# Kernel tuning notes

Measured on AMD Instinct MI355X. Metric: run time of the kernel, lower is better.

## Reference

```python
import jax, jax.numpy as jnp
import numpy as np

B, NX, NC, D, H = 2, 512, 4096, 1024, 16
HD = D // H  # head_dim = context_dim // heads
LN_EPS = 1e-5


def setup_inputs() -> dict:
    key = jax.random.key(0)
    k0, k1, k2, k3, k4 = jax.random.split(key, 5)
    x = jax.random.normal(k0, (B, NX, D), dtype=jnp.float32)
    c = jax.random.normal(k1, (B, NC, D), dtype=jnp.float32)
    attn_mask = jax.random.randint(k2, (B, NX, NC), 0, 2).astype(bool)
    # learned params
    ln_w = jnp.ones((D,), jnp.float32)
    ln_b = jnp.zeros((D,), jnp.float32)
    Wq = jax.random.normal(k3, (D, D), dtype=jnp.float32) * 0.02  # to_q (query_dim -> inner_dim)
    Wo = jax.random.normal(k4, (D, D), dtype=jnp.float32) * 0.02  # to_out (inner_dim -> query_dim)
    return {"x": x, "c": c, "attn_mask": attn_mask, "ln_w": ln_w, "ln_b": ln_b, "Wq": Wq, "Wo": Wo}


def _layernorm(x, w, b):
    mu = jnp.mean(x, axis=-1, keepdims=True)
    var = jnp.mean(jnp.square(x - mu), axis=-1, keepdims=True)
    return (x - mu) * jax.lax.rsqrt(var + LN_EPS) * w + b


def reference(x, c, attn_mask, ln_w, ln_b, Wq, Wo):
    scale = HD ** (-0.5)
    xn = _layernorm(x, ln_w, ln_b)
    q = (xn @ Wq).reshape(B, NX, H, HD).transpose(0, 2, 1, 3)      # (B,H,NX,HD)
    kv0 = c.reshape(B, NC, H, HD).transpose(0, 2, 1, 3)             # (B,H,NC,HD) -- kvt=(kv0,kv0)
    kv = jnp.concatenate([q, kv0], axis=2)                          # kv_append_q=True -> (B,H,NX+NC,HD)
    # mask: ones for the appended-q block, user mask for context block
    m = jnp.broadcast_to(attn_mask[:, None, :, :], (B, H, NX, NC))
    full_mask = jnp.concatenate([jnp.ones((B, H, NX, NX), bool), m], axis=-1)
    sim = jnp.einsum('bhqd,bhkd->bhqk', q * scale, kv)              # (B,H,NX,NX+NC)
    neg = -jnp.finfo(sim.dtype).max
    sim = jnp.where(full_mask, sim, neg)
    attn = jax.nn.softmax(sim, axis=-1)
    a = jnp.einsum('bhqk,bhkd->bhqd', attn, kv)
    o = a.transpose(0, 2, 1, 3).reshape(B, NX, H * HD) @ Wo
    return (o, kv0)
```

## Files before the change

### kernel.cpp

```cpp
#include <hip/hip_runtime.h>

#define B_  2
#define NX_ 512
#define NC_ 4096
#define D_  1024
#define H_  16
#define HD_ 64
#define NT_ (NX_ + NC_)
#define NSPLIT 4
#define KBS (NT_ / 64 / NSPLIT)

typedef float  floatx4  __attribute__((ext_vector_type(4)));
typedef __bf16 bf16x8   __attribute__((ext_vector_type(8)));
typedef unsigned short ushort8v __attribute__((ext_vector_type(8)));

__device__ __forceinline__ bf16x8 as_bf16x8(ushort8v u) {
    union { ushort8v u; bf16x8 b; } c; c.u = u; return c.b;
}
__device__ __forceinline__ unsigned short f2bf(float f) {
    unsigned u = __float_as_uint(f);
    u += 0x7FFF + ((u >> 16) & 1);
    return (unsigned short)(u >> 16);
}

__global__ __launch_bounds__(256)
void prep_kernel(const float* __restrict__ x, const float* __restrict__ lw,
                 const float* __restrict__ lb, const float* __restrict__ Wq,
                 const float* __restrict__ Wo, const int* __restrict__ mask,
                 const float* __restrict__ c,
                 unsigned short* __restrict__ xnb, unsigned short* __restrict__ WqT,
                 unsigned short* __restrict__ WoT, unsigned* __restrict__ bits,
                 unsigned short* __restrict__ cbf, float* __restrict__ gz) {
    int blk = blockIdx.x;
    int tid = threadIdx.x;
    if (blk < 1024) {
        int row = blk;
        float4 v = reinterpret_cast<const float4*>(x)[(size_t)row * (D_ / 4) + tid];
        float s  = v.x + v.y + v.z + v.w;
        float s2 = v.x * v.x + v.y * v.y + v.z * v.z + v.w * v.w;
        #pragma unroll
        for (int off = 32; off > 0; off >>= 1) {
            s  += __shfl_down(s, off);
            s2 += __shfl_down(s2, off);
        }
        __shared__ float sm[4], sm2[4], stat[2];
        int wv = tid >> 6;
        if ((tid & 63) == 0) { sm[wv] = s; sm2[wv] = s2; }
        __syncthreads();
        if (tid == 0) {
            float S  = sm[0] + sm[1] + sm[2] + sm[3];
            float S2 = sm2[0] + sm2[1] + sm2[2] + sm2[3];
            float mu  = S * (1.0f / D_);
            float var = fmaxf(S2 * (1.0f / D_) - mu * mu, 0.0f);
            stat[0] = mu;
            stat[1] = rsqrtf(var + 1e-5f);
        }
        __syncthreads();
        float mu = stat[0], rs = stat[1];
        float4 w4 = reinterpret_cast<const float4*>(lw)[tid];
        float4 b4 = reinterpret_cast<const float4*>(lb)[tid];
        ushort4 o;
        o.x = f2bf((v.x - mu) * rs * w4.x + b4.x);
        o.y = f2bf((v.y - mu) * rs * w4.y + b4.y);
        o.z = f2bf((v.z - mu) * rs * w4.z + b4.z);
        o.w = f2bf((v.w - mu) * rs * w4.w + b4.w);
        reinterpret_cast<ushort4*>(xnb)[(size_t)row * (D_ / 4) + tid] = o;
    } else if (blk < 1536) {
        int which = (blk - 1024) >> 8;
        int t = (blk - 1024) & 255;
        const float* W = which ? Wo : Wq;
        unsigned short* WT = which ? WoT : WqT;
        __shared__ unsigned short T[64][72];
        int row0 = (t >> 4) * 64, col0 = (t & 15) * 64;
        int r = tid >> 2, ch = (tid & 3) * 16;
        const float* src = W + (size_t)(row0 + r) * D_ + col0 + ch;
        unsigned short vals[16];
        #pragma unroll
        for (int k = 0; k < 4; ++k) {
            float4 v = reinterpret_cast<const float4*>(src)[k];
            vals[k*4+0] = f2bf(v.x); vals[k*4+1] = f2bf(v.y);
            vals[k*4+2] = f2bf(v.z); vals[k*4+3] = f2bf(v.w);
        }
        #pragma unroll
        for (int i = 0; i < 16; ++i) T[ch + i][r] = vals[i];
        __syncthreads();
        unsigned short* dst = WT + (size_t)(col0 + r) * D_ + row0 + ch;
        uint4 o0 = *reinterpret_cast<uint4*>(&T[r][ch]);
        uint4 o1 = *reinterpret_cast<uint4*>(&T[r][ch + 8]);
        *reinterpret_cast<uint4*>(dst)     = o0;
        *reinterpret_cast<uint4*>(dst + 8) = o1;
    } else if (blk < 2048) {
        size_t w = (size_t)(blk - 1536) * 256 + tid;
        const int* src = mask + w * 32;
        unsigned b = 0;
        #pragma unroll
        for (int k = 0; k < 8; ++k) {
            int4 v = reinterpret_cast<const int4*>(src)[k];
            b |= (v.x != 0 ? 1u : 0u) << (k * 4 + 0);
            b |= (v.y != 0 ? 1u : 0u) << (k * 4 + 1);
            b |= (v.z != 0 ? 1u : 0u) << (k * 4 + 2);
            b |= (v.w != 0 ? 1u : 0u) << (k * 4 + 3);
        }
        bits[w] = b;
    } else if (blk < 10240) {
        size_t i = ((size_t)(blk - 2048) * 256 + tid) * 4;
        float4 v = *reinterpret_cast<const float4*>(c + i);
        ushort4 o;
        o.x = f2bf(v.x); o.y = f2bf(v.y); o.z = f2bf(v.z); o.w = f2bf(v.w);
        *reinterpret_cast<ushort4*>(cbf + i) = o;
    } else {
        size_t i = ((size_t)(blk - 10240) * 256 + tid) * 4;
        float4 z = {0.f, 0.f, 0.f, 0.f};
        *reinterpret_cast<float4*>(gz + i) = z;
    }
}

__global__ __launch_bounds__(256)
void kv0_kernel(const float* __restrict__ c, float* __restrict__ out2) {
    size_t i = (size_t)blockIdx.x * 256 + threadIdx.x;
    int d4 = (int)(i & 15);
    size_t r = i >> 4;
    int n = (int)(r % NC_);
    size_t r2 = r / NC_;
    int h = (int)(r2 & (H_ - 1));
    int b = (int)(r2 >> 4);
    float4 v = *reinterpret_cast<const float4*>(c + ((size_t)(b * NC_ + n)) * D_ + h * HD_ + d4 * 4);
    reinterpret_cast<float4*>(out2)[i] = v;
}

__global__ __launch_bounds__(256)
void gemm_bt_kernel(const unsigned short* __restrict__ A, const unsigned short* __restrict__ BT,
                    unsigned short* __restrict__ Cb) {
    __shared__ unsigned short As[64][72];
    __shared__ unsigned short Bs[64][72];
    int tid = threadIdx.x;
    int lane = tid & 63, wave = tid >> 6;
    int m16 = lane & 15, g = lane >> 4, g8 = g * 8;
    int row0 = blockIdx.y * 64, col0 = blockIdx.x * 64;
    int r = tid >> 2, ch = (tid & 3) * 16;

    floatx4 acc[4];
    #pragma unroll
    for (int t = 0; t < 4; ++t) acc[t] = (floatx4){0.f, 0.f, 0.f, 0.f};

    for (int kc = 0; kc < 16; ++kc) {
        int k0 = kc * 64;
        const unsigned short* asrc = A  + (size_t)(row0 + r) * D_ + k0 + ch;
        const unsigned short* bsrc = BT + (size_t)(col0 + r) * D_ + k0 + ch;
        uint4 a0 = *reinterpret_cast<const uint4*>(asrc);
        uint4 a1 = *reinterpret_cast<const uint4*>(asrc + 8);
        uint4 b0 = *reinterpret_cast<const uint4*>(bsrc);
        uint4 b1 = *reinterpret_cast<const uint4*>(bsrc + 8);
        *reinterpret_cast<uint4*>(&As[r][ch])     = a0;
        *reinterpret_cast<uint4*>(&As[r][ch + 8]) = a1;
        *reinterpret_cast<uint4*>(&Bs[r][ch])     = b0;
        *reinterpret_cast<uint4*>(&Bs[r][ch + 8]) = b1;
        __syncthreads();
        bf16x8 fa0 = as_bf16x8(*reinterpret_cast<ushort8v*>(&As[16 * wave + m16][g8]));
        bf16x8 fa1 = as_bf16x8(*reinterpret_cast<ushort8v*>(&As[16 * wave + m16][32 + g8]));
        #pragma unroll
        for (int t = 0; t < 4; ++t) {
            bf16x8 fb0 = as_bf16x8(*reinterpret_cast<ushort8v*>(&Bs[16 * t + m16][g8]));
            bf16x8 fb1 = as_bf16x8(*reinterpret_cast<ushort8v*>(&Bs[16 * t + m16][32 + g8]));
            acc[t] = __builtin_amdgcn_mfma_f32_16x16x32_bf16(fa0, fb0, acc[t], 0, 0, 0);
            acc[t] = __builtin_amdgcn_mfma_f32_16x16x32_bf16(fa1, fb1, acc[t], 0, 0, 0);
        }
        __syncthreads();
    }
    #pragma unroll
    for (int t = 0; t < 4; ++t)
        #pragma unroll
        for (int reg = 0; reg < 4; ++reg)
            Cb[(size_t)(row0 + 16 * wave + g * 4 + reg) * D_ + col0 + 16 * t + m16] = f2bf(acc[t][reg]);
}

__global__ __launch_bounds__(256)
void gemm_attn_kernel(const float* __restrict__ gacc, const float* __restrict__ gacc_l,
                      const unsigned short* __restrict__ BT, float* __restrict__ out) {
    __shared__ unsigned short As[64][72];
    __shared__ unsigned short Bs[64][72];
    int tid = threadIdx.x;
    int lane = tid & 63, wave = tid >> 6;
    int m16 = lane & 15, g = lane >> 4, g8 = g * 8;
    int row0 = blockIdx.y * 64, col0 = blockIdx.x * 64;
    int r = tid >> 2, ch = (tid & 3) * 16;

    floatx4 acc[4];
    #pragma unroll
    for (int t = 0; t < 4; ++t) acc[t] = (floatx4){0.f, 0.f, 0.f, 0.f};

    for (int kc = 0; kc < 16; ++kc) {
        int k0 = kc * 64;
        int row = row0 + r;
        float inv = 1.0f / fmaxf(gacc_l[(size_t)row * H_ + kc], 1e-35f);
        const float* asrc = gacc + (size_t)row * D_ + k0 + ch;
        const unsigned short* bsrc = BT + (size_t)(col0 + r) * D_ + k0 + ch;
        unsigned short av[16];
        #pragma unroll
        for (int t = 0; t < 4; ++t) {
            float4 v = reinterpret_cast<const float4*>(asrc)[t];
            av[t*4+0] = f2bf(v.x * inv); av[t*4+1] = f2bf(v.y * inv);
            av[t*4+2] = f2bf(v.z * inv); av[t*4+3] = f2bf(v.w * inv);
        }
        uint4 b0 = *reinterpret_cast<const uint4*>(bsrc);
        uint4 b1 = *reinterpret_cast<const uint4*>(bsrc + 8);
        *reinterpret_cast<uint4*>(&As[r][ch])     = *reinterpret_cast<uint4*>(&av[0]);
        *reinterpret_cast<uint4*>(&As[r][ch + 8]) = *reinterpret_cast<uint4*>(&av[8]);
        *reinterpret_cast<uint4*>(&Bs[r][ch])     = b0;
        *reinterpret_cast<uint4*>(&Bs[r][ch + 8]) = b1;
        __syncthreads();
        bf16x8 fa0 = as_bf16x8(*reinterpret_cast<ushort8v*>(&As[16 * wave + m16][g8]));
        bf16x8 fa1 = as_bf16x8(*reinterpret_cast<ushort8v*>(&As[16 * wave + m16][32 + g8]));
        #pragma unroll
        for (int t = 0; t < 4; ++t) {
            bf16x8 fb0 = as_bf16x8(*reinterpret_cast<ushort8v*>(&Bs[16 * t + m16][g8]));
            bf16x8 fb1 = as_bf16x8(*reinterpret_cast<ushort8v*>(&Bs[16 * t + m16][32 + g8]));
            acc[t] = __builtin_amdgcn_mfma_f32_16x16x32_bf16(fa0, fb0, acc[t], 0, 0, 0);
            acc[t] = __builtin_amdgcn_mfma_f32_16x16x32_bf16(fa1, fb1, acc[t], 0, 0, 0);
        }
        __syncthreads();
    }
    #pragma unroll
    for (int t = 0; t < 4; ++t)
        #pragma unroll
        for (int reg = 0; reg < 4; ++reg)
            out[(size_t)(row0 + 16 * wave + g * 4 + reg) * D_ + col0 + 16 * t + m16] = acc[t][reg];
}

__global__ __launch_bounds__(256, 4)
void attn_kernel(const unsigned short* __restrict__ qbf,
                 const unsigned short* __restrict__ cbf,
                 const unsigned* __restrict__ maskbits,
                 float* __restrict__ gacc, float* __restrict__ gacc_l) {
    int blk   = blockIdx.x;
    int bh    = ((blk >> 8) << 3) | (blk & 7);
    int inner = (blk >> 3) & 31;
    int qt    = inner & 7;
    int split = inner >> 3;
    int h  = bh & 15;
    int b  = bh >> 4;
    int tid  = threadIdx.x;
    int lane = tid & 63;
    int wave = tid >> 6;
    int m16  = lane & 15;
    int g    = lane >> 4;
    int g8   = g * 8;

    __shared__ unsigned short Ks [64][72];
    __shared__ unsigned short Kts[64][72];
    __shared__ unsigned short Ps [64][64];

    const unsigned short* qrow = qbf + ((size_t)(b * NX_ + qt * 64 + 16 * wave + m16)) * D_ + h * HD_;
    bf16x8 qa0 = as_bf16x8(*reinterpret_cast<const ushort8v*>(qrow + g8));
    bf16x8 qa1 = as_bf16x8(*reinterpret_cast<const ushort8v*>(qrow + 32 + g8));

    floatx4 acc_o[4];
    #pragma unroll
    for (int td = 0; td < 4; ++td) acc_o[td] = (floatx4){0.f, 0.f, 0.f, 0.f};
    float l_acc[4] = {0.f, 0.f, 0.f, 0.f};

    int keyl = tid >> 2, dch = (tid & 3) * 16;
    int prsw = 2 * ((m16 >> 2) & 3);

    for (int i = 0; i < KBS; ++i) {
        int kb = split * KBS + i;
        __syncthreads();
        const unsigned short* src = (kb < 8)
            ? qbf + ((size_t)(b * NX_ + kb * 64 + keyl)) * D_ + h * HD_ + dch
            : cbf + ((size_t)(b * NC_ + kb * 64 - NX_ + keyl)) * D_ + h * HD_ + dch;
        union { uint4 v[2]; unsigned short s[16]; } u;
        u.v[0] = *reinterpret_cast<const uint4*>(src);
        u.v[1] = *reinterpret_cast<const uint4*>(src + 8);
        *reinterpret_cast<uint4*>(&Ks[keyl][dch])     = u.v[0];
        *reinterpret_cast<uint4*>(&Ks[keyl][dch + 8]) = u.v[1];
        #pragma unroll
        for (int k = 0; k < 16; ++k) {
            int d = dch + k;
            int pc = ((keyl >> 3) + (d >> 3)) & 7;
            Kts[d][pc * 8 + (keyl & 7)] = u.s[k];
        }
        __syncthreads();

        floatx4 accs[4];
        #pragma unroll
        for (int t = 0; t < 4; ++t) {
            bf16x8 b0 = as_bf16x8(*reinterpret_cast<ushort8v*>(&Ks[16 * t + m16][g8]));
            bf16x8 b1 = as_bf16x8(*reinterpret_cast<ushort8v*>(&Ks[16 * t + m16][32 + g8]));
            floatx4 d = (floatx4){0.f, 0.f, 0.f, 0.f};
            d = __builtin_amdgcn_mfma_f32_16x16x32_bf16(qa0, b0, d, 0, 0, 0);
            d = __builtin_amdgcn_mfma_f32_16x16x32_bf16(qa1, b1, d, 0, 0, 0);
            accs[t] = d;
        }

        unsigned mw0[4], mw1[4];
        if (kb >= 8) {
            #pragma unroll
            for (int r = 0; r < 4; ++r) {
                size_t mi = ((size_t)(b * NX_ + qt * 64 + 16 * wave + g * 4 + r)) * (NC_ / 32)
                          + (size_t)(kb - 8) * 2;
                uint2 w = *reinterpret_cast<const uint2*>(&maskbits[mi]);
                mw0[r] = w.x; mw1[r] = w.y;
            }
        }

        float psum[4] = {0.f, 0.f, 0.f, 0.f};
        #pragma unroll
        for (int t = 0; t < 4; ++t) {
            int cc = 2 * t + (m16 >> 3);
            #pragma unroll
            for (int r = 0; r < 4; ++r) {
                float s = accs[t][r] * 0.125f;
                float p = __expf(fminf(s, 64.0f) - 64.0f);
                if (kb >= 8) {
                    unsigned w = (t < 2) ? mw0[r] : mw1[r];
                    unsigned bit = (w >> ((16 * t + m16) & 31)) & 1u;
                    p = bit ? p : 0.0f;
                }
                psum[r] += p;
                int prow = 16 * wave + g * 4 + r;
                int pc = (cc + 2 * g) & 7;
                Ps[prow][pc * 8 + (m16 & 7)] = f2bf(p);
            }
        }
        #pragma unroll
        for (int r = 0; r < 4; ++r) {
            float v = psum[r];
            v += __shfl_xor(v, 1, 16);
            v += __shfl_xor(v, 2, 16);
            v += __shfl_xor(v, 4, 16);
            v += __shfl_xor(v, 8, 16);
            l_acc[r] += v;
        }
        asm volatile("s_waitcnt lgkmcnt(0)" ::: "memory");

        bf16x8 p0 = as_bf16x8(*reinterpret_cast<ushort8v*>(&Ps[16 * wave + m16][((g + prsw) & 7) * 8]));
        bf16x8 p1 = as_bf16x8(*reinterpret_cast<ushort8v*>(&Ps[16 * wave + m16][((4 + g + prsw) & 7) * 8]));
        #pragma unroll
        for (int td = 0; td < 4; ++td) {
            int row = 16 * td + m16;
            int rh = row >> 3;
            bf16x8 v0 = as_bf16x8(*reinterpret_cast<ushort8v*>(&Kts[row][((g + rh) & 7) * 8]));
            bf16x8 v1 = as_bf16x8(*reinterpret_cast<ushort8v*>(&Kts[row][((4 + g + rh) & 7) * 8]));
            acc_o[td] = __builtin_amdgcn_mfma_f32_16x16x32_bf16(p0, v0, acc_o[td], 0, 0, 0);
            acc_o[td] = __builtin_amdgcn_mfma_f32_16x16x32_bf16(p1, v1, acc_o[td], 0, 0, 0);
        }
    }

    #pragma unroll
    for (int r = 0; r < 4; ++r) {
        int qrow_ = qt * 64 + 16 * wave + g * 4 + r;
        float* dst = gacc + ((size_t)(b * NX_ + qrow_)) * D_ + h * HD_;
        #pragma unroll
        for (int td = 0; td < 4; ++td)
            unsafeAtomicAdd(&dst[16 * td + m16], acc_o[td][r]);
        if (m16 == 0)
            unsafeAtomicAdd(&gacc_l[(size_t)(b * NX_ + qrow_) * H_ + h], l_acc[r]);
    }
}

extern "C" void kernel_launch(void* const* d_in, const int* in_sizes, int n_in,
                              void* d_out, int out_size, void* d_ws, size_t ws_size,
                              hipStream_t stream) {
    (void)in_sizes; (void)n_in; (void)out_size; (void)d_ws; (void)ws_size;
    const float* x    = (const float*)d_in[0];
    const float* c    = (const float*)d_in[1];
    const int*   mask = (const int*)d_in[2];
    const float* ln_w = (const float*)d_in[3];
    const float* ln_b = (const float*)d_in[4];
    const float* Wq   = (const float*)d_in[5];
    const float* Wo   = (const float*)d_in[6];
    float* out  = (float*)d_out;
    float* out2 = out + (size_t)B_ * NX_ * D_;

    float* base = out2;
    unsigned short* qbf      = (unsigned short*)(base);
    unsigned*       maskbits = (unsigned*)(base + 524288);
    float*          gacc     = base + 655360;
    float*          gacc_l   = base + 1703936;
    unsigned short* WqT      = (unsigned short*)(base + 1720320);
    unsigned short* WoT      = (unsigned short*)(base + 2244608);
    unsigned short* xnb      = (unsigned short*)(base + 2768896);
    unsigned short* cbf      = (unsigned short*)(base + 3817472);

    prep_kernel<<<11280, 256, 0, stream>>>(x, ln_w, ln_b, Wq, Wo, mask, c,
                                           xnb, WqT, WoT, maskbits, cbf, gacc);
    gemm_bt_kernel<<<dim3(16, 16), 256, 0, stream>>>(xnb, WqT, qbf);
    attn_kernel<<<NSPLIT * 256, 256, 0, stream>>>(qbf, cbf, maskbits, gacc, gacc_l);
    gemm_attn_kernel<<<dim3(16, 16), 256, 0, stream>>>(gacc, gacc_l, WoT, out);
    kv0_kernel<<<(B_ * H_ * NC_ * HD_ / 4) / 256, 256, 0, stream>>>(c, out2);
}
```

Before: 223.0 us.

## Restructure K tile transpose, use exp2, and compute row sums via MFMA

Each thread now loads a 4x4 key/dim block with 8-byte loads and builds the transposed K tile using byte-permute instructions, replacing the 16 scalar LDS stores per thread. Softmax probabilities use hardware exp2 with the scale and log2e folded into one constant. The bf16 conversion is now truncation instead of round-to-nearest. Row sums are accumulated by an MFMA against a ones vector instead of shuffle reductions, which also makes the normaliser consistent with the bf16 P values actually used. The costs are that global loads become narrower, and truncation adds a slight bias to P.

```diff
diff --git a/kernel.cpp b/kernel.cpp
--- a/kernel.cpp
+++ b/kernel.cpp
@@ -257,27 +257,42 @@
     floatx4 acc_o[4];
     #pragma unroll
     for (int td = 0; td < 4; ++td) acc_o[td] = (floatx4){0.f, 0.f, 0.f, 0.f};
-    float l_acc[4] = {0.f, 0.f, 0.f, 0.f};
-
-    int keyl = tid >> 2, dch = (tid & 3) * 16;
+    floatx4 acc_l = (floatx4){0.f, 0.f, 0.f, 0.f};
+
+    ushort8v ones_u;
+    #pragma unroll
+    for (int j = 0; j < 8; ++j) ones_u[j] = 0x3F80;
+    bf16x8 onesf = as_bf16x8(ones_u);
+
+    int Kg = tid >> 4;
+    int Dg = tid & 15;
+    int pcst = ((Kg >> 1) + (Dg >> 1)) & 7;
     int prsw = 2 * ((m16 >> 2) & 3);
 
     for (int i = 0; i < KBS; ++i) {
         int kb = split * KBS + i;
         __syncthreads();
         const unsigned short* src = (kb < 8)
-            ? qbf + ((size_t)(b * NX_ + kb * 64 + keyl)) * D_ + h * HD_ + dch
-            : cbf + ((size_t)(b * NC_ + kb * 64 - NX_ + keyl)) * D_ + h * HD_ + dch;
-        union { uint4 v[2]; unsigned short s[16]; } u;
-        u.v[0] = *reinterpret_cast<const uint4*>(src);
-        u.v[1] = *reinterpret_cast<const uint4*>(src + 8);
-        *reinterpret_cast<uint4*>(&Ks[keyl][dch])     = u.v[0];
-        *reinterpret_cast<uint4*>(&Ks[keyl][dch + 8]) = u.v[1];
-        #pragma unroll
-        for (int k = 0; k < 16; ++k) {
-            int d = dch + k;
-            int pc = ((keyl >> 3) + (d >> 3)) & 7;
-            Kts[d][pc * 8 + (keyl & 7)] = u.s[k];
+            ? qbf + ((size_t)(b * NX_ + kb * 64 + 4 * Kg)) * D_ + h * HD_ + 4 * Dg
+            : cbf + ((size_t)(b * NC_ + kb * 64 - NX_ + 4 * Kg)) * D_ + h * HD_ + 4 * Dg;
+        uint2 rows[4];
+        #pragma unroll
+        for (int kk = 0; kk < 4; ++kk)
+            rows[kk] = *reinterpret_cast<const uint2*>(src + (size_t)kk * D_);
+        #pragma unroll
+        for (int kk = 0; kk < 4; ++kk)
+            *reinterpret_cast<uint2*>(&Ks[4 * Kg + kk][4 * Dg]) = rows[kk];
+        #pragma unroll
+        for (int i2 = 0; i2 < 4; ++i2) {
+            unsigned sel = (i2 & 1) ? 0x07060302u : 0x05040100u;
+            unsigned r0 = (i2 >> 1) ? rows[0].y : rows[0].x;
+            unsigned r1 = (i2 >> 1) ? rows[1].y : rows[1].x;
+            unsigned r2 = (i2 >> 1) ? rows[2].y : rows[2].x;
+            unsigned r3 = (i2 >> 1) ? rows[3].y : rows[3].x;
+            uint2 cw;
+            cw.x = __builtin_amdgcn_perm(r1, r0, sel);
+            cw.y = __builtin_amdgcn_perm(r3, r2, sel);
+            *reinterpret_cast<uint2*>(&Kts[4 * Dg + i2][pcst * 8 + 4 * (Kg & 1)]) = cw;
         }
         __syncthreads();
 
@@ -303,38 +318,31 @@
             }
         }
 
-        float psum[4] = {0.f, 0.f, 0.f, 0.f};
+        const float C1 = 0.18033688011112042f;
+        const float C2 = 92.33248261689366f;
         #pragma unroll
         for (int t = 0; t < 4; ++t) {
             int cc = 2 * t + (m16 >> 3);
             #pragma unroll
             for (int r = 0; r < 4; ++r) {
-                float s = accs[t][r] * 0.125f;
-                float p = __expf(fminf(s, 64.0f) - 64.0f);
+                float e = fminf(accs[t][r] * C1, C2) - C2;
+                float p = __builtin_amdgcn_exp2f(e);
                 if (kb >= 8) {
                     unsigned w = (t < 2) ? mw0[r] : mw1[r];
                     unsigned bit = (w >> ((16 * t + m16) & 31)) & 1u;
                     p = bit ? p : 0.0f;
                 }
-                psum[r] += p;
                 int prow = 16 * wave + g * 4 + r;
                 int pc = (cc + 2 * g) & 7;
-                Ps[prow][pc * 8 + (m16 & 7)] = f2bf(p);
+                Ps[prow][pc * 8 + (m16 & 7)] = (unsigned short)(__float_as_uint(p) >> 16);
             }
-        }
-        #pragma unroll
-        for (int r = 0; r < 4; ++r) {
-            float v = psum[r];
-            v += __shfl_xor(v, 1, 16);
-            v += __shfl_xor(v, 2, 16);
-            v += __shfl_xor(v, 4, 16);
-            v += __shfl_xor(v, 8, 16);
-            l_acc[r] += v;
         }
         asm volatile("s_waitcnt lgkmcnt(0)" ::: "memory");
 
         bf16x8 p0 = as_bf16x8(*reinterpret_cast<ushort8v*>(&Ps[16 * wave + m16][((g + prsw) & 7) * 8]));
         bf16x8 p1 = as_bf16x8(*reinterpret_cast<ushort8v*>(&Ps[16 * wave + m16][((4 + g + prsw) & 7) * 8]));
+        acc_l = __builtin_amdgcn_mfma_f32_16x16x32_bf16(p0, onesf, acc_l, 0, 0, 0);
+        acc_l = __builtin_amdgcn_mfma_f32_16x16x32_bf16(p1, onesf, acc_l, 0, 0, 0);
         #pragma unroll
         for (int td = 0; td < 4; ++td) {
             int row = 16 * td + m16;
@@ -354,7 +362,7 @@
         for (int td = 0; td < 4; ++td)
             unsafeAtomicAdd(&dst[16 * td + m16], acc_o[td][r]);
         if (m16 == 0)
-            unsafeAtomicAdd(&gacc_l[(size_t)(b * NX_ + qrow_) * H_ + h], l_acc[r]);
+            unsafeAtomicAdd(&gacc_l[(size_t)(b * NX_ + qrow_) * H_ + h], acc_l[r]);
     }
 }
 
```

Measured after the change: 205.6 us. 1.08x faster.
